# Optimization experiments

Hardware: AMD Instinct MI355X
Metric: run time of the kernel (lower is better)

Reference implementation:

```python
import jax, jax.numpy as jnp
import numpy as np
from jax import lax


def _interp_matrix(n_in: int, n_out: int) -> jnp.ndarray:
    """Row-stochastic [n_out, n_in] matrix for 1-D linear interp, align_corners=True."""
    if n_in == 1:
        return jnp.ones((n_out, 1), dtype=jnp.float32)
    pos = jnp.arange(n_out, dtype=jnp.float32) * ((n_in - 1) / (n_out - 1))
    lo = jnp.clip(jnp.floor(pos).astype(jnp.int32), 0, n_in - 2)
    frac = pos - lo.astype(jnp.float32)
    rows = jnp.arange(n_out)
    W = jnp.zeros((n_out, n_in), dtype=jnp.float32)
    W = W.at[rows, lo].add(1.0 - frac)
    W = W.at[rows, lo + 1].add(frac)
    return W


def setup_inputs() -> dict:
    key = jax.random.key(0)
    ks = jax.random.split(key, 10)
    B, C, H, W = 8, 64, 128, 128
    Ch = C // 2
    x = jax.random.normal(ks[0], (B, C, H, W), dtype=jnp.float32)
    # fan-in scaled weights to keep softmax logits in a sane range
    pool_w = jax.random.normal(ks[1], (C, C, 3, 3), dtype=jnp.float32) / np.sqrt(C * 9)
    pool_b = jax.random.normal(ks[2], (C,), dtype=jnp.float32) * 0.1
    q_w = jax.random.normal(ks[3], (Ch, C), dtype=jnp.float32) / np.sqrt(C)
    q_b = jax.random.normal(ks[4], (Ch,), dtype=jnp.float32) * 0.1
    k_w = jax.random.normal(ks[5], (Ch, C), dtype=jnp.float32) / np.sqrt(C)
    k_b = jax.random.normal(ks[6], (Ch,), dtype=jnp.float32) * 0.1
    v_w = jax.random.normal(ks[7], (C, C), dtype=jnp.float32) / np.sqrt(C)
    v_b = jax.random.normal(ks[8], (C,), dtype=jnp.float32) * 0.1
    gamma = jax.random.normal(ks[9], (1,), dtype=jnp.float32)
    return {"x": x, "pool_w": pool_w, "pool_b": pool_b, "q_w": q_w, "q_b": q_b,
            "k_w": k_w, "k_b": k_b, "v_w": v_w, "v_b": v_b, "gamma": gamma}


def reference(x, pool_w, pool_b, q_w, q_b, k_w, k_b, v_w, v_b, gamma):
    # 3x3 stride-2 pad-1 conv (the 'pool')
    xp = lax.conv_general_dilated(x, pool_w, window_strides=(2, 2),
                                  padding=((1, 1), (1, 1)),
                                  dimension_numbers=('NCHW', 'OIHW', 'NCHW'))
    xp = xp + pool_b[None, :, None, None]
    B, C, h, w = xp.shape
    N = h * w
    xf = xp.reshape(B, C, N)  # [B, C, N]
    # 1x1 convs as matmuls over the channel dim
    q = jnp.einsum('oc,bcn->bon', q_w, xf) + q_b[None, :, None]   # [B, C/2, N]
    k = jnp.einsum('oc,bcn->bon', k_w, xf) + k_b[None, :, None]   # [B, C/2, N]
    v = jnp.einsum('oc,bcn->bon', v_w, xf) + v_b[None, :, None]   # [B, C, N]
    # energy[b, n, m] = <q[:, n], k[:, m]>  -> softmax over m
    energy = jnp.einsum('bdn,bdm->bnm', q, k)                     # [B, N, N]
    attn = jax.nn.softmax(energy, axis=-1)
    # out = value @ attention^T  (torch: bmm(v, attn.permute(0,2,1)))
    out = jnp.einsum('bcm,bnm->bcn', v, attn).reshape(B, C, h, w)
    out = gamma[0] * out
    # bilinear upsample to input size, align_corners=True (separable matmuls)
    H, Wd = x.shape[2], x.shape[3]
    Wh = _interp_matrix(h, H)
    Ww = _interp_matrix(w, Wd)
    out = jnp.einsum('Hh,bchw->bcHw', Wh, out)
    out = jnp.einsum('Ww,bchw->bchW', Ww, out)
    return out + x
```

## Files before the change

kernel.cpp:

```cpp
#include <hip/hip_runtime.h>


typedef __attribute__((ext_vector_type(8))) short bf16x8;
typedef __attribute__((ext_vector_type(4))) float f32x4;

#define DEV static __device__ __forceinline__

DEV unsigned f2bf(float f) {
  union { float f; unsigned u; } a; a.f = f;
  return (a.u + 0x7FFFu + ((a.u >> 16) & 1u)) >> 16;
}
DEV float u2f(unsigned u) { union { unsigned u; float f; } a; a.u = u; return a.f; }
DEV unsigned cvtpk(float lo, float hi) {
  unsigned r;
  asm("v_cvt_pk_bf16_f32 %0, %1, %2" : "=v"(r) : "v"(lo), "v"(hi));
  return r;
}
DEV bf16x8 mk_bf16x8(unsigned w0, unsigned w1, unsigned w2, unsigned w3) {
  union { unsigned u[4]; bf16x8 v; } x;
  x.u[0] = w0; x.u[1] = w1; x.u[2] = w2; x.u[3] = w3;
  return x.v;
}
DEV void gload_lds16(const void* g, void* l) {
  __builtin_amdgcn_global_load_lds(
      (const __attribute__((address_space(1))) void*)g,
      (__attribute__((address_space(3))) void*)l, 16, 0, 0);
}

__global__ __launch_bounds__(256) void prep_kernel(
    const float* __restrict__ pw, const float* __restrict__ qw,
    const float* __restrict__ kw, const float* __restrict__ vw,
    const float* __restrict__ qb, const float* __restrict__ kb,
    const float* __restrict__ vb,
    unsigned short* __restrict__ Ag, unsigned short* __restrict__ A2g,
    float* __restrict__ bias2) {
  const float LOG2E = 1.4426950408889634f;
  const int i = blockIdx.x * 256 + threadIdx.x;
  if (i < 36864) {
    const int oc = i / 576, k = i - oc * 576;
    const int tap = k >> 6, ic = k & 63;
    Ag[i] = (unsigned short)f2bf(pw[(oc * 64 + ic) * 9 + tap]);
  }
  const int j = i - 36864;
  if (j >= 0 && j < 8192) {
    const int r = j >> 6, c = j & 63;
    if (r < 32)       A2g[j] = (unsigned short)f2bf(qw[r * 64 + c] * LOG2E);
    else if (r < 64)  A2g[j] = (unsigned short)f2bf(kw[(r - 32) * 64 + c]);
    else              A2g[j] = (unsigned short)f2bf(vw[(r - 64) * 64 + c]);
  }
  if (j >= 8192 && j < 8320) {
    const int r = j - 8192;
    bias2[r] = r < 32 ? qb[r] * LOG2E : (r < 64 ? kb[r - 32] : vb[r - 64]);
  }
}

__global__ __launch_bounds__(256) void convqkv_kernel(
    const float* __restrict__ x, const unsigned short* __restrict__ Ag,
    const float* __restrict__ pool_b, const unsigned short* __restrict__ A2g,
    const float* __restrict__ bias2,
    unsigned short* __restrict__ qT, unsigned short* __restrict__ kT,
    unsigned short* __restrict__ vM) {
  const int b = blockIdx.x >> 6, oy = blockIdx.x & 63;
  const int t = threadIdx.x, w = t >> 6, lane = t & 63;
  const int lr = lane & 15, lg = lane >> 4;
  __shared__ unsigned short sIn[390 * 64];
  __shared__ unsigned short sXP[64 * 64];
  char* sInB = (char*)sIn;
  char* sXPB = (char*)sXP;

  bf16x8 af[18];
  {
    const unsigned short* ap = Ag + (w * 16 + lr) * 576 + (lg << 3);
    #pragma unroll
    for (int kc = 0; kc < 18; ++kc)
      af[kc] = *(const bf16x8*)(ap + kc * 32);
  }

  #pragma unroll
  for (int rr = 0; rr < 2; ++rr) {
    const int pos = t + rr * 256;
    if (pos < 390) {
      const int ky = pos / 130, xi = pos - ky * 130;
      const int iy = 2 * oy + ky - 1, ix = xi - 1;
      const bool ok = (iy >= 0) & (iy < 128) & (ix >= 0) & (ix < 128);
      const float* xs = x + ((size_t)(b * 64) * 128 + (ok ? iy : 0)) * 128 +
                        (ok ? ix : 0);
      const int sw = pos & 7;
      #pragma unroll
      for (int o = 0; o < 8; ++o) {
        float f[8];
        #pragma unroll
        for (int jj = 0; jj < 8; ++jj)
          f[jj] = ok ? xs[(size_t)(o * 8 + jj) * 16384] : 0.f;
        bf16x8 v = mk_bf16x8(cvtpk(f[0], f[1]), cvtpk(f[2], f[3]),
                             cvtpk(f[4], f[5]), cvtpk(f[6], f[7]));
        *(bf16x8*)(sInB + pos * 128 + ((o ^ sw) << 4)) = v;
      }
    }
  }
  __syncthreads();

  f32x4 acc[4];
  #pragma unroll
  for (int nt = 0; nt < 4; ++nt) acc[nt] = (f32x4){0.f, 0.f, 0.f, 0.f};
  #pragma unroll
  for (int kc = 0; kc < 18; ++kc) {
    const int tap = kc >> 1, ky = tap / 3, kx = tap - ky * 3;
    const int o = ((kc & 1) << 2) + lg;
    #pragma unroll
    for (int nt = 0; nt < 4; ++nt) {
      const int xi = 2 * (nt * 16 + lr) + kx;
      const int pos = ky * 130 + xi;
      bf16x8 bfr = *(const bf16x8*)(sInB + pos * 128 + ((o ^ (pos & 7)) << 4));
      acc[nt] = __builtin_amdgcn_mfma_f32_16x16x32_bf16(af[kc], bfr, acc[nt],
                                                        0, 0, 0);
    }
  }

  const int ocBase = w * 16 + (lg << 2);
  float pb[4];
  #pragma unroll
  for (int r = 0; r < 4; ++r) pb[r] = pool_b[ocBase + r];
  const int ocOct = ocBase >> 3;
  const int withinB = (ocBase & 7) * 2;
  #pragma unroll
  for (int nt = 0; nt < 4; ++nt) {
    const int pos = nt * 16 + lr;
    const unsigned p01 = cvtpk(acc[nt][0] + pb[0], acc[nt][1] + pb[1]);
    const unsigned p23 = cvtpk(acc[nt][2] + pb[2], acc[nt][3] + pb[3]);
    char* base = sXPB + pos * 128 + ((ocOct ^ (pos & 7)) << 4) + withinB;
    *(unsigned*)(base) = p01;
    *(unsigned*)(base + 4) = p23;
  }
  __syncthreads();

  bf16x8 a2[2][2];
  #pragma unroll
  for (int mt = 0; mt < 2; ++mt)
    #pragma unroll
    for (int kc2 = 0; kc2 < 2; ++kc2)
      a2[mt][kc2] = *(const bf16x8*)(A2g + ((2 * w + mt) * 16 + lr) * 64 +
                                     kc2 * 32 + (lg << 3));
  f32x4 acc2[2][4];
  #pragma unroll
  for (int mt = 0; mt < 2; ++mt)
    #pragma unroll
    for (int nt = 0; nt < 4; ++nt) acc2[mt][nt] = (f32x4){0.f, 0.f, 0.f, 0.f};
  #pragma unroll
  for (int kc2 = 0; kc2 < 2; ++kc2) {
    const int o2 = (kc2 << 2) + lg;
    #pragma unroll
    for (int nt = 0; nt < 4; ++nt) {
      const int pos = nt * 16 + lr;
      bf16x8 bfr = *(const bf16x8*)(sXPB + pos * 128 + ((o2 ^ (pos & 7)) << 4));
      acc2[0][nt] = __builtin_amdgcn_mfma_f32_16x16x32_bf16(a2[0][kc2], bfr,
                                                            acc2[0][nt], 0, 0, 0);
      acc2[1][nt] = __builtin_amdgcn_mfma_f32_16x16x32_bf16(a2[1][kc2], bfr,
                                                            acc2[1][nt], 0, 0, 0);
    }
  }

  const int n0g = oy << 6;
  #pragma unroll
  for (int mt = 0; mt < 2; ++mt) {
    const int rowB = (2 * w + mt) * 16 + (lg << 2);
    float b2[4];
    #pragma unroll
    for (int r = 0; r < 4; ++r) b2[r] = bias2[rowB + r];
    if (rowB < 32) {
      #pragma unroll
      for (int nt = 0; nt < 4; ++nt) {
        const int n = n0g + nt * 16 + lr;
        unsigned* dst = (unsigned*)(qT + (((size_t)(b << 12) + n) << 5) + rowB);
        dst[0] = cvtpk(acc2[mt][nt][0] + b2[0], acc2[mt][nt][1] + b2[1]);
        dst[1] = cvtpk(acc2[mt][nt][2] + b2[2], acc2[mt][nt][3] + b2[3]);
      }
    } else if (rowB < 64) {
      #pragma unroll
      for (int nt = 0; nt < 4; ++nt) {
        const int n = n0g + nt * 16 + lr;
        unsigned* dst = (unsigned*)(kT + (((size_t)(b << 12) + n) << 5) + rowB - 32);
        dst[0] = cvtpk(acc2[mt][nt][0] + b2[0], acc2[mt][nt][1] + b2[1]);
        dst[1] = cvtpk(acc2[mt][nt][2] + b2[2], acc2[mt][nt][3] + b2[3]);
      }
    } else {
      const int cv = rowB - 64;
      #pragma unroll
      for (int nt = 0; nt < 4; ++nt) {
        const int n = n0g + nt * 16 + lr;
        #pragma unroll
        for (int r = 0; r < 4; ++r)
          vM[(((size_t)(b << 6) + cv + r) << 12) + n] =
              (unsigned short)f2bf(acc2[mt][nt][r] + b2[r]);
      }
    }
  }
}

__global__ __launch_bounds__(256, 2) void attn_kernel(
    const unsigned short* __restrict__ qT, const unsigned short* __restrict__ kT,
    const unsigned short* __restrict__ vM,
    unsigned short* __restrict__ Pb, float* __restrict__ Lbuf) {
  __shared__ char lds[36864];
  const int t = threadIdx.x, w = t >> 6, lane = t & 63;
  const int lr = lane & 15, lg = lane >> 4;
  const int b = blockIdx.x & 7;
  const int u = (blockIdx.x >> 3) & 15;
  const int s = blockIdx.x >> 7;
  const int n0 = (u << 8) + (w << 6);
  const int kb0 = s << 10;

  bf16x8 bq[4];
  #pragma unroll
  for (int nt = 0; nt < 4; ++nt)
    bq[nt] = *(const bf16x8*)(
        qT + (((size_t)(b << 12) + n0 + nt * 16 + lr) << 5) + (lg << 3));

  const unsigned short* ksrc = kT + ((size_t)b << 17);
  const unsigned short* vsrcb = vM + ((size_t)b << 18);

  f32x4 acc[4][4];
  #pragma unroll
  for (int nt = 0; nt < 4; ++nt)
    #pragma unroll
    for (int ct = 0; ct < 4; ++ct) acc[nt][ct] = (f32x4){0.f, 0.f, 0.f, 0.f};
  float l_run[4] = {0.f, 0.f, 0.f, 0.f};

  const int s0 = lr + ((lane & 16) << 1);
  const int s1 = s0 + 16;
  const bool hi = (lane & 32) != 0;
  const int vsw = (lane & 7) ^ ((lane >> 3) & 7);

  #define STAGE(ci_) {                                                         \
    const int kb_ = kb0 + (((ci_) & 15) << 6);                                 \
    char* sb_ = lds + ((ci_) % 3) * 12288;                                     \
    gload_lds16((const void*)(ksrc +                                           \
                  (((size_t)(kb_ + (w << 4) + (lane >> 2))) << 5) +            \
                  ((lane & 3) << 3)),                                          \
                sb_ + (w << 10));                                              \
    gload_lds16((const void*)(vsrcb +                                          \
                  (((size_t)((w << 4) + (lane >> 3))) << 12) + kb_ +           \
                  (vsw << 3)),                                                 \
                sb_ + 4096 + (w << 11));                                       \
    gload_lds16((const void*)(vsrcb +                                          \
                  (((size_t)((w << 4) + 8 + (lane >> 3))) << 12) + kb_ +       \
                  (vsw << 3)),                                                 \
                sb_ + 4096 + (w << 11) + 1024);                                \
  }

  STAGE(0);
  STAGE(1);

  for (int cc = 0; cc < 16; ++cc) {
    STAGE(cc + 2);
    asm volatile("s_waitcnt vmcnt(6)" ::: "memory");
    __builtin_amdgcn_s_barrier();
    __builtin_amdgcn_sched_barrier(0);
    char* base = lds + (cc % 3) * 12288;

    f32x4 st[4][4];
    const f32x4 z4 = {0.f, 0.f, 0.f, 0.f};
    __builtin_amdgcn_s_setprio(1);
    #pragma unroll
    for (int j = 0; j < 4; ++j) {
      const bf16x8 ka = *(const bf16x8*)(base + ((16 * j + lr) << 6) + (lg << 4));
      #pragma unroll
      for (int nt = 0; nt < 4; ++nt)
        st[nt][j] = __builtin_amdgcn_mfma_f32_16x16x32_bf16(ka, bq[nt], z4,
                                                            0, 0, 0);
    }
    __builtin_amdgcn_s_setprio(0);

    unsigned pw_[4][4][2];
    #pragma unroll
    for (int nt = 0; nt < 4; ++nt) {
      float ps0 = 0.f, ps1 = 0.f;
      #pragma unroll
      for (int j = 0; j < 4; ++j) {
        const float p0 = __builtin_amdgcn_exp2f(st[nt][j][0]);
        const float p1 = __builtin_amdgcn_exp2f(st[nt][j][1]);
        const float p2 = __builtin_amdgcn_exp2f(st[nt][j][2]);
        const float p3 = __builtin_amdgcn_exp2f(st[nt][j][3]);
        ps0 += p0 + p1;
        ps1 += p2 + p3;
        pw_[nt][j][0] = cvtpk(p0, p1);
        pw_[nt][j][1] = cvtpk(p2, p3);
      }
      l_run[nt] += ps0 + ps1;
    }

    #pragma unroll
    for (int h = 0; h < 2; ++h) {
      bf16x8 pbv[4];
      #pragma unroll
      for (int nt = 0; nt < 4; ++nt) {
        const int f0 = 2 * h, f1 = 2 * h + 1;
        const unsigned a0 = __shfl((int)pw_[nt][f0][0], s0, 64);
        const unsigned a1 = __shfl((int)pw_[nt][f0][1], s0, 64);
        const unsigned a2 = __shfl((int)pw_[nt][f0][0], s1, 64);
        const unsigned a3 = __shfl((int)pw_[nt][f0][1], s1, 64);
        const unsigned c0 = __shfl((int)pw_[nt][f1][0], s0, 64);
        const unsigned c1 = __shfl((int)pw_[nt][f1][1], s0, 64);
        const unsigned c2 = __shfl((int)pw_[nt][f1][0], s1, 64);
        const unsigned c3 = __shfl((int)pw_[nt][f1][1], s1, 64);
        pbv[nt] = hi ? mk_bf16x8(c0, c1, c2, c3) : mk_bf16x8(a0, a1, a2, a3);
      }
      __builtin_amdgcn_s_setprio(1);
      #pragma unroll
      for (int ct = 0; ct < 4; ++ct) {
        const int c = (ct << 4) + lr;
        const int o = (h << 2) + lg;
        const bf16x8 va = *(const bf16x8*)(
            base + 4096 + (c << 7) + ((o ^ (lr & 7)) << 4));
        #pragma unroll
        for (int nt = 0; nt < 4; ++nt)
          acc[nt][ct] = __builtin_amdgcn_mfma_f32_16x16x32_bf16(va, pbv[nt],
                                                                acc[nt][ct],
                                                                0, 0, 0);
      }
      __builtin_amdgcn_s_setprio(0);
    }

    __builtin_amdgcn_sched_barrier(0);
    asm volatile("s_waitcnt lgkmcnt(0)" ::: "memory");
    __builtin_amdgcn_s_barrier();
  }

  #pragma unroll
  for (int nt = 0; nt < 4; ++nt) {
    l_run[nt] += __shfl_xor(l_run[nt], 16, 64);
    l_run[nt] += __shfl_xor(l_run[nt], 32, 64);
  }

  unsigned short* dst = Pb + ((size_t)s << 21);
  #pragma unroll
  for (int nt = 0; nt < 4; ++nt) {
    const int q = n0 + nt * 16 + lr;
    #pragma unroll
    for (int ct = 0; ct < 4; ++ct)
      #pragma unroll
      for (int r = 0; r < 4; ++r) {
        const int c = (ct << 4) + (lg << 2) + r;
        dst[((size_t)((b << 6) + c) << 12) + q] =
            (unsigned short)f2bf(acc[nt][ct][r]);
      }
  }
  if (lane < 16) {
    #pragma unroll
    for (int nt = 0; nt < 4; ++nt)
      Lbuf[((size_t)(s * 8 + b) << 12) + n0 + nt * 16 + lane] = l_run[nt];
  }
}

__global__ __launch_bounds__(256) void merge_kernel(
    const unsigned short* __restrict__ Pb, const float* __restrict__ Lbuf,
    const float* __restrict__ gamma_p, float* __restrict__ attnP) {
  const int idx = blockIdx.x * 256 + threadIdx.x;
  const int n0 = (idx & 511) << 3;
  const int c = (idx >> 9) & 63;
  const int b = idx >> 15;
  const size_t base = ((size_t)((b << 6) + c) << 12) + n0;

  float num[8] = {0.f, 0.f, 0.f, 0.f, 0.f, 0.f, 0.f, 0.f};
  #pragma unroll
  for (int s = 0; s < 4; ++s) {
    const uint4 v = *(const uint4*)(Pb + ((size_t)s << 21) + base);
    num[0] += u2f(v.x << 16); num[1] += u2f(v.x & 0xffff0000u);
    num[2] += u2f(v.y << 16); num[3] += u2f(v.y & 0xffff0000u);
    num[4] += u2f(v.z << 16); num[5] += u2f(v.z & 0xffff0000u);
    num[6] += u2f(v.w << 16); num[7] += u2f(v.w & 0xffff0000u);
  }
  float den[8] = {0.f, 0.f, 0.f, 0.f, 0.f, 0.f, 0.f, 0.f};
  #pragma unroll
  for (int s = 0; s < 4; ++s) {
    const float* lp = Lbuf + (((size_t)(s * 8 + b)) << 12) + n0;
    const f32x4 l0 = *(const f32x4*)lp;
    const f32x4 l1 = *(const f32x4*)(lp + 4);
    #pragma unroll
    for (int j = 0; j < 4; ++j) { den[j] += l0[j]; den[4 + j] += l1[j]; }
  }
  const float g = gamma_p[0];
  f32x4 o0, o1;
  #pragma unroll
  for (int j = 0; j < 4; ++j) {
    o0[j] = g * num[j] / den[j];
    o1[j] = g * num[4 + j] / den[4 + j];
  }
  *(f32x4*)(attnP + base) = o0;
  *(f32x4*)(attnP + base + 4) = o1;
}

__global__ __launch_bounds__(256) void upsample_residual_kernel(
    const float* __restrict__ attn_out, const float* __restrict__ x,
    float* __restrict__ out) {
  const int idx = blockIdx.x * 256 + threadIdx.x;
  const int X0 = (idx & 31) << 2;
  int rem = idx >> 5;
  const int Y = rem & 127; rem >>= 7;
  const int c = rem & 63;
  const int b = rem >> 6;

  const float sr = 63.0f / 127.0f;
  float fy = Y * sr;
  int iy = (int)fy; if (iy > 62) iy = 62;
  const float ty = fy - (float)iy;
  const float* ap = attn_out + (((size_t)(b * 64 + c)) << 12);
  const float* r0 = ap + iy * 64;
  const float* r1 = r0 + 64;

  float tmp[4];
  #pragma unroll
  for (int k = 0; k < 4; ++k) {
    const int X = X0 + k;
    float fx = X * sr;
    int ix = (int)fx; if (ix > 62) ix = 62;
    const float tx = fx - (float)ix;
    float v0 = r0[ix] + tx * (r0[ix + 1] - r0[ix]);
    float v1 = r1[ix] + tx * (r1[ix + 1] - r1[ix]);
    tmp[k] = v0 + ty * (v1 - v0);
  }
  const size_t o = (((size_t)((b * 64 + c) * 128 + Y)) << 7) + X0;
  f32x4 xv = *reinterpret_cast<const f32x4*>(x + o);
  f32x4 ov = {tmp[0] + xv[0], tmp[1] + xv[1], tmp[2] + xv[2], tmp[3] + xv[3]};
  *reinterpret_cast<f32x4*>(out + o) = ov;
}

extern "C" void kernel_launch(void* const* d_in, const int* in_sizes, int n_in,
                              void* d_out, int out_size, void* d_ws, size_t ws_size,
                              hipStream_t stream) {
  const float* x      = (const float*)d_in[0];
  const float* pool_w = (const float*)d_in[1];
  const float* pool_b = (const float*)d_in[2];
  const float* q_w    = (const float*)d_in[3];
  const float* q_b    = (const float*)d_in[4];
  const float* k_w    = (const float*)d_in[5];
  const float* k_b    = (const float*)d_in[6];
  const float* v_w    = (const float*)d_in[7];
  const float* v_b    = (const float*)d_in[8];
  const float* gamma  = (const float*)d_in[9];
  float* out = (float*)d_out;

  char* ws = (char*)d_ws;
  unsigned short* Ag   = (unsigned short*)(ws);
  unsigned short* A2g  = (unsigned short*)(ws + 81920);
  float* bias2         = (float*)(ws + 98304);
  unsigned short* qT   = (unsigned short*)(ws + 1048576);
  unsigned short* kT   = (unsigned short*)(ws + 3145728);
  unsigned short* vM   = (unsigned short*)(ws + 5242880);
  unsigned short* Pb   = (unsigned short*)(ws + 9437184);
  float* Lbuf          = (float*)(ws + 26214400);
  float* attnP         = (float*)(ws + 1048576);

  prep_kernel<<<177, 256, 0, stream>>>(pool_w, q_w, k_w, v_w, q_b, k_b, v_b,
                                       Ag, A2g, bias2);
  convqkv_kernel<<<512, 256, 0, stream>>>(x, Ag, pool_b, A2g, bias2, qT, kT, vM);
  attn_kernel<<<512, 256, 0, stream>>>(qT, kT, vM, Pb, Lbuf);
  merge_kernel<<<1024, 256, 0, stream>>>(Pb, Lbuf, gamma, attnP);
  upsample_residual_kernel<<<8192, 256, 0, stream>>>(attnP, x, out);
}
```

Before: 99.35 us.

## Split attention keys eight ways, swizzle K LDS layout, single barrier per chunk

Templates the attention and merge kernels on the number of key splits and launches 1024 blocks with an 8-way split when the workspace is large enough, with launch bounds raised to four blocks per SIMD. This is meant to raise occupancy and parallelism. The K tile in LDS is now XOR-swizzled to avoid bank conflicts. The pipeline issues the next stage after the barrier and drops the trailing barrier, leaving one sync per chunk. The cost is double the partial-sum traffic in the merge, and the tighter register budget from the new launch bound may cause spills.

After: 186.4 us. 87.6% more time.

```diff
diff --git a/kernel.cpp b/kernel.cpp
--- a/kernel.cpp
+++ b/kernel.cpp
@@ -197,10 +197,12 @@
   }
 }
 
-__global__ __launch_bounds__(256, 2) void attn_kernel(
+template <int NSPLIT>
+__global__ __launch_bounds__(256, 4) void attn_kernel(
     const unsigned short* __restrict__ qT, const unsigned short* __restrict__ kT,
     const unsigned short* __restrict__ vM,
     unsigned short* __restrict__ Pb, float* __restrict__ Lbuf) {
+  constexpr int CH = 64 / NSPLIT;
   __shared__ char lds[36864];
   const int t = threadIdx.x, w = t >> 6, lane = t & 63;
   const int lr = lane & 15, lg = lane >> 4;
@@ -208,7 +210,7 @@
   const int u = (blockIdx.x >> 3) & 15;
   const int s = blockIdx.x >> 7;
   const int n0 = (u << 8) + (w << 6);
-  const int kb0 = s << 10;
+  const int kb0 = s * (CH << 6);
 
   bf16x8 bq[4];
   #pragma unroll
@@ -230,13 +232,14 @@
   const int s1 = s0 + 16;
   const bool hi = (lane & 32) != 0;
   const int vsw = (lane & 7) ^ ((lane >> 3) & 7);
+  const int klocal = (w << 4) + (lane >> 2);
+  const int kseg = (lane & 3) ^ ((klocal >> 1) & 3);
 
   #define STAGE(ci_) {                                                         \
-    const int kb_ = kb0 + (((ci_) & 15) << 6);                                 \
+    const int kb_ = kb0 + (((ci_) & (CH - 1)) << 6);                           \
     char* sb_ = lds + ((ci_) % 3) * 12288;                                     \
-    gload_lds16((const void*)(ksrc +                                           \
-                  (((size_t)(kb_ + (w << 4) + (lane >> 2))) << 5) +            \
-                  ((lane & 3) << 3)),                                          \
+    gload_lds16((const void*)(ksrc + (((size_t)(kb_ + klocal)) << 5) +         \
+                  (kseg << 3)),                                                \
                 sb_ + (w << 10));                                              \
     gload_lds16((const void*)(vsrcb +                                          \
                   (((size_t)((w << 4) + (lane >> 3))) << 12) + kb_ +           \
@@ -251,11 +254,11 @@
   STAGE(0);
   STAGE(1);
 
-  for (int cc = 0; cc < 16; ++cc) {
-    STAGE(cc + 2);
-    asm volatile("s_waitcnt vmcnt(6)" ::: "memory");
+  for (int cc = 0; cc < CH; ++cc) {
+    asm volatile("s_waitcnt vmcnt(3)" ::: "memory");
     __builtin_amdgcn_s_barrier();
     __builtin_amdgcn_sched_barrier(0);
+    STAGE(cc + 2);
     char* base = lds + (cc % 3) * 12288;
 
     f32x4 st[4][4];
@@ -263,7 +266,9 @@
     __builtin_amdgcn_s_setprio(1);
     #pragma unroll
     for (int j = 0; j < 4; ++j) {
-      const bf16x8 ka = *(const bf16x8*)(base + ((16 * j + lr) << 6) + (lg << 4));
+      const int key = 16 * j + lr;
+      const bf16x8 ka = *(const bf16x8*)(
+          base + (key << 6) + ((lg ^ ((key >> 1) & 3)) << 4));
       #pragma unroll
       for (int nt = 0; nt < 4; ++nt)
         st[nt][j] = __builtin_amdgcn_mfma_f32_16x16x32_bf16(ka, bq[nt], z4,
@@ -320,10 +325,6 @@
       }
       __builtin_amdgcn_s_setprio(0);
     }
-
-    __builtin_amdgcn_sched_barrier(0);
-    asm volatile("s_waitcnt lgkmcnt(0)" ::: "memory");
-    __builtin_amdgcn_s_barrier();
   }
 
   #pragma unroll
@@ -350,8 +351,10 @@
     for (int nt = 0; nt < 4; ++nt)
       Lbuf[((size_t)(s * 8 + b) << 12) + n0 + nt * 16 + lane] = l_run[nt];
   }
-}
-
+  #undef STAGE
+}
+
+template <int NSPLIT>
 __global__ __launch_bounds__(256) void merge_kernel(
     const unsigned short* __restrict__ Pb, const float* __restrict__ Lbuf,
     const float* __restrict__ gamma_p, float* __restrict__ attnP) {
@@ -363,7 +366,7 @@
 
   float num[8] = {0.f, 0.f, 0.f, 0.f, 0.f, 0.f, 0.f, 0.f};
   #pragma unroll
-  for (int s = 0; s < 4; ++s) {
+  for (int s = 0; s < NSPLIT; ++s) {
     const uint4 v = *(const uint4*)(Pb + ((size_t)s << 21) + base);
     num[0] += u2f(v.x << 16); num[1] += u2f(v.x & 0xffff0000u);
     num[2] += u2f(v.y << 16); num[3] += u2f(v.y & 0xffff0000u);
@@ -372,7 +375,7 @@
   }
   float den[8] = {0.f, 0.f, 0.f, 0.f, 0.f, 0.f, 0.f, 0.f};
   #pragma unroll
-  for (int s = 0; s < 4; ++s) {
+  for (int s = 0; s < NSPLIT; ++s) {
     const float* lp = Lbuf + (((size_t)(s * 8 + b)) << 12) + n0;
     const f32x4 l0 = *(const f32x4*)lp;
     const f32x4 l1 = *(const f32x4*)(lp + 4);
@@ -448,13 +451,20 @@
   unsigned short* kT   = (unsigned short*)(ws + 3145728);
   unsigned short* vM   = (unsigned short*)(ws + 5242880);
   unsigned short* Pb   = (unsigned short*)(ws + 9437184);
-  float* Lbuf          = (float*)(ws + 26214400);
   float* attnP         = (float*)(ws + 1048576);
 
   prep_kernel<<<177, 256, 0, stream>>>(pool_w, q_w, k_w, v_w, q_b, k_b, v_b,
                                        Ag, A2g, bias2);
   convqkv_kernel<<<512, 256, 0, stream>>>(x, Ag, pool_b, A2g, bias2, qT, kT, vM);
-  attn_kernel<<<512, 256, 0, stream>>>(qT, kT, vM, Pb, Lbuf);
-  merge_kernel<<<1024, 256, 0, stream>>>(Pb, Lbuf, gamma, attnP);
+
+  if (ws_size >= 44040192u) {
+    float* Lbuf = (float*)(ws + 9437184 + 8 * 4194304);
+    attn_kernel<8><<<1024, 256, 0, stream>>>(qT, kT, vM, Pb, Lbuf);
+    merge_kernel<8><<<1024, 256, 0, stream>>>(Pb, Lbuf, gamma, attnP);
+  } else {
+    float* Lbuf = (float*)(ws + 9437184 + 4 * 4194304);
+    attn_kernel<4><<<512, 256, 0, stream>>>(qT, kT, vM, Pb, Lbuf);
+    merge_kernel<4><<<1024, 256, 0, stream>>>(Pb, Lbuf, gamma, attnP);
+  }
   upsample_residual_kernel<<<8192, 256, 0, stream>>>(attnP, x, out);
 }
```
